# Kernel tuning notes

Hardware: AMD Instinct MI355X
Metric: run time of the kernel (lower is better)

## Reference

```python
import jax, jax.numpy as jnp
import numpy as np

B = 512       # batch_size
IN = 256      # input_size
H = 512       # hidden_size
OUT = 64      # output_size
N_PAIRS = B - 1   # number of H0 persistence deaths (connected components merges)
TOL = 1e-6    # rtol for torch.isclose
ATOL = 1e-8   # torch default atol
EPS = 0.0     # homology_eps
TARGET_P = 1.0
HOM_P = 1.0
COMP_P = 0.01

_IU = np.triu_indices(B, 1)  # condensed pdist indexing, static


def _mlp(batch, W1, b1, W2, b2, W3, b3, Wout, bout):
    # FeedForward: input->hidden, (n_layers-1) hidden->hidden, hidden->output, ReLU
    h = jax.nn.relu(batch @ W1 + b1)
    h = jax.nn.relu(h @ W2 + b2)
    h = jax.nn.relu(h @ W3 + b3)
    return h @ Wout + bout


def _pdist(y):
    # condensed euclidean pairwise distances, same ordering as torch F.pdist
    d = y[_IU[0]] - y[_IU[1]]                 # [P, OUT]
    return jnp.sqrt(jnp.sum(d * d, axis=-1))  # [P]


def setup_inputs() -> dict:
    key = jax.random.key(0)
    ks = jax.random.split(key, 8)
    batch = jax.random.normal(ks[0], (B, IN), jnp.float32)
    target = jax.random.normal(ks[1], (B, OUT), jnp.float32)
    W1 = jax.random.normal(ks[2], (IN, H), jnp.float32) / np.sqrt(IN)
    W2 = jax.random.normal(ks[3], (H, H), jnp.float32) / np.sqrt(H)
    W3 = jax.random.normal(ks[4], (H, H), jnp.float32) / np.sqrt(H)
    Wout = jax.random.normal(ks[5], (H, OUT), jnp.float32) / np.sqrt(H)
    b1 = jnp.zeros((H,), jnp.float32)
    b2 = jnp.zeros((H,), jnp.float32)
    b3 = jnp.zeros((H,), jnp.float32)
    bout = jnp.zeros((OUT,), jnp.float32)
    # persistence deaths = actual critical pdist values (from the external
    # Vietoris-Rips routine in the original); sample N_PAIRS distinct entries.
    y0 = _mlp(batch, W1, b1, W2, b2, W3, b3, Wout, bout)
    pd0 = np.asarray(_pdist(y0))
    idx = np.random.default_rng(0).choice(pd0.shape[0], N_PAIRS, replace=False)
    persistence_deaths = jnp.asarray(pd0[idx], jnp.float32)
    return {"batch": batch, "target": target,
            "W1": W1, "b1": b1, "W2": W2, "b2": b2, "W3": W3, "b3": b3,
            "Wout": Wout, "bout": bout,
            "persistence_deaths": persistence_deaths}


def reference(batch, target, W1, b1, W2, b2, W3, b3, Wout, bout, persistence_deaths):
    y = _mlp(batch, W1, b1, W2, b2, W3, b3, Wout, bout)   # [B, OUT]
    y_hom = y  # normalize_for_homology = False
    pd = _pdist(y_hom)                                     # [P]
    # vectorized indicator_death over all pairs (replaces per-pair Python loop)
    mask = jnp.any(jnp.isclose(pd[:, None], persistence_deaths[None, :],
                               rtol=TOL, atol=ATOL), axis=1)      # [P] bool
    # homology_dim=0: birth_pdist = 0; norm=1 of selected (death - 0 + eps)
    homology_loss = jnp.sum(jnp.abs(jnp.where(mask, pd + EPS, 0.0)))
    target_loss = jnp.mean((target - y) ** 2)
    compactness_loss = jnp.sum(jnp.abs(y - jnp.mean(y, axis=0, keepdims=True)))
    loss = TARGET_P * target_loss + HOM_P * homology_loss + COMP_P * compactness_loss
    return loss
```

## Files before the change

### kernel.cpp

```cpp
#include <hip/hip_runtime.h>

#define B_    512
#define IN_   256
#define H_    512
#define OUT_  64
#define NDEATH (B_ - 1)
#define NSORT  512
#define RTOL_ 1e-6
#define ATOL_ 1e-8
#define NBLK  256
#define NTHR  512
#define KT    32

typedef __attribute__((ext_vector_type(4))) double d4_t;

__device__ __forceinline__ void ast(double* p, double v) {
    __hip_atomic_store(p, v, __ATOMIC_RELAXED, __HIP_MEMORY_SCOPE_AGENT);
}
__device__ __forceinline__ double ald(const double* p) {
    return __hip_atomic_load(p, __ATOMIC_RELAXED, __HIP_MEMORY_SCOPE_AGENT);
}
__device__ __forceinline__ unsigned aldu(const unsigned* p) {
    return __hip_atomic_load(p, __ATOMIC_RELAXED, __HIP_MEMORY_SCOPE_AGENT);
}
__device__ __forceinline__ void aadd(unsigned* p) {
    __hip_atomic_fetch_add(p, 1u, __ATOMIC_RELAXED, __HIP_MEMORY_SCOPE_AGENT);
}

__device__ __forceinline__ void lbar() {
    asm volatile("s_waitcnt lgkmcnt(0)" ::: "memory");
    __builtin_amdgcn_s_barrier();
    asm volatile("" ::: "memory");
}

__device__ __forceinline__ void gbar(unsigned* cnt, unsigned nb) {
    __syncthreads();
    if (threadIdx.x == 0) {
        aadd(cnt);
        while (aldu(cnt) < nb) __builtin_amdgcn_s_sleep(1);
    }
    __syncthreads();
}

__device__ __forceinline__ void gbar2(unsigned* gslot, unsigned* root,
                                      int leader) {
    __syncthreads();
    if (threadIdx.x == 0) {
        aadd(gslot);
        if (leader) {
            while (aldu(gslot) < 16u) __builtin_amdgcn_s_sleep(1);
            aadd(root);
        }
        while (aldu(root) < 16u) __builtin_amdgcn_s_sleep(1);
    }
    __syncthreads();
}

__device__ void sort_windows(const float* __restrict__ deaths,
                             double* sd, double* slo, double* shi, int t) {
    if (t < NSORT) sd[t] = (t < NDEATH) ? (double)deaths[t] : 1e300;
    __syncthreads();
    for (int k = 2; k <= NSORT; k <<= 1) {
        for (int j = k >> 1; j > 0; j >>= 1) {
            if (t < 256) {
                int l = ((t & ~(j - 1)) << 1) | (t & (j - 1));
                int p = l + j;
                bool up = ((l & k) == 0);
                double a = sd[l], b = sd[p];
                if ((a > b) == up) { sd[l] = b; sd[p] = a; }
            }
            __syncthreads();
        }
    }
    if (t < NSORT) {
        double d = sd[t];
        double w = ATOL_ + RTOL_ * fabs(d);
        slo[t] = d - w;
        shi[t] = d + w;
    }
    __syncthreads();
}

template <typename TIN, bool RELU>
__device__ void gemm_dev(const TIN* __restrict__ A, const float* __restrict__ W,
                         const float* __restrict__ bias, double* __restrict__ C,
                         int N, int K, int tile, int t,
                         double (&As)[2][2][KT][33]) {
    const int lane  = t & 63;
    const int wave4 = (t >> 6) & 3;
    const int w2    = t >> 8;
    const int tg    = t & 255;
    const int wm    = wave4 & 1, wn = wave4 >> 1;
    const int nbx   = N >> 5;
    const int row0  = (tile / nbx) << 5;
    const int col0  = (tile % nbx) << 5;

    const int akk   = tg & 31;
    const int amm   = tg >> 5;
    const int kbase = w2 * (K >> 1);
    const int nkt   = K >> 6;

    const int mrow  = wm * 16 + (lane & 15);
    const int ncol  = wn * 16 + (lane & 15);
    const int kq    = lane >> 4;

    TIN   ar[3][4];
    float br[3][8];

    auto load_a = [&](int rs, int kt) {
        const int k0 = kbase + (kt << 5);
        #pragma unroll
        for (int p = 0; p < 4; ++p)
            ar[rs][p] = A[(size_t)(row0 + amm + 8 * p) * K + k0 + akk];
    };
    auto load_b = [&](int rs, int kt) {
        const int k0 = kbase + (kt << 5);
        const float* wp = W + (size_t)(k0 + kq) * N + col0 + ncol;
        #pragma unroll
        for (int ks = 0; ks < 8; ++ks)
            br[rs][ks] = wp[(size_t)(4 * ks) * N];
    };
    auto stage_a = [&](int rs, int buf) {
        #pragma unroll
        for (int p = 0; p < 4; ++p)
            As[w2][buf][akk][amm + 8 * p] = (double)ar[rs][p];
    };

    load_a(0, 0); load_b(0, 0);
    if (nkt > 1) { load_a(1, 1); load_b(1, 1); }
    if (nkt > 2) { load_a(2, 2); load_b(2, 2); }
    stage_a(0, 0);
    lbar();

    d4_t c4a = {0.0, 0.0, 0.0, 0.0};
    d4_t c4b = {0.0, 0.0, 0.0, 0.0};

    for (int kt = 0; kt < nkt; ++kt) {
        const int cur = kt & 1;
        const int rs  = kt % 3;
        #pragma unroll
        for (int ks = 0; ks < 4; ++ks) {
            double av = As[w2][cur][ks * 4 + kq][mrow];
            c4a = __builtin_amdgcn_mfma_f64_16x16x4f64(av, (double)br[rs][ks],
                                                       c4a, 0, 0, 0);
        }
        #pragma unroll
        for (int ks = 4; ks < 8; ++ks) {
            double av = As[w2][cur][ks * 4 + kq][mrow];
            c4b = __builtin_amdgcn_mfma_f64_16x16x4f64(av, (double)br[rs][ks],
                                                       c4b, 0, 0, 0);
        }
        if (kt + 3 < nkt) { load_a(rs, kt + 3); load_b(rs, kt + 3); }
        if (kt + 1 < nkt) stage_a((kt + 1) % 3, cur ^ 1);
        lbar();
    }

    d4_t c4 = c4a + c4b;

    double (*cEx)[16][17] = (double (*)[16][17])(&As[0][0][0][0]);
    const int r4 = (lane >> 4) * 4;
    if (w2 == 1) {
        #pragma unroll
        for (int r = 0; r < 4; ++r)
            cEx[wave4][r4 + r][lane & 15] = c4[r];
    }
    lbar();
    if (w2 == 0) {
        #pragma unroll
        for (int r = 0; r < 4; ++r) {
            int row = row0 + wm * 16 + r4 + r;
            int col = col0 + wn * 16 + (lane & 15);
            double v = c4[r] + cEx[wave4][r4 + r][lane & 15] + (double)bias[col];
            if (RELU) v = v > 0.0 ? v : 0.0;
            ast(&C[(size_t)row * N + col], v);
        }
    }
}

__device__ void mc_dev(const float* __restrict__ target,
                       const double* __restrict__ y,
                       double* __restrict__ t_part, double* __restrict__ c_part,
                       int c, int t) {
    const int wave = t >> 6, lane = t & 63;
    double v = y[(size_t)t * OUT_ + c];
    double s = v;
    for (int off = 32; off; off >>= 1) s += __shfl_down(s, off);
    __shared__ double swm[8];
    __shared__ double smean;
    if (lane == 0) swm[wave] = s;
    __syncthreads();
    if (t == 0) {
        double m = 0.0;
        #pragma unroll
        for (int w = 0; w < 8; ++w) m += swm[w];
        smean = m / (double)B_;
    }
    __syncthreads();
    double m = smean;
    double d = (double)target[(size_t)t * OUT_ + c] - v;
    double t_s = d * d;
    double c_s = fabs(v - m);
    for (int off = 32; off; off >>= 1) {
        t_s += __shfl_down(t_s, off);
        c_s += __shfl_down(c_s, off);
    }
    __shared__ double st[8], sc[8];
    if (lane == 0) { st[wave] = t_s; sc[wave] = c_s; }
    __syncthreads();
    if (t == 0) {
        double ts = 0.0, cs = 0.0;
        #pragma unroll
        for (int w = 0; w < 8; ++w) { ts += st[w]; cs += sc[w]; }
        ast(&t_part[c], ts);
        ast(&c_part[c], cs);
    }
}

__device__ __forceinline__ double pair_val(const double* __restrict__ yrow_s,
                                           const double* __restrict__ yj,
                                           const double* __restrict__ slo,
                                           const double* __restrict__ shi) {
    double s = 0.0;
    #pragma unroll
    for (int d = 0; d < OUT_; d += 2) {
        double2 v = *(const double2*)(yj + d);
        double d0 = yrow_s[d]     - v.x;
        double d1 = yrow_s[d + 1] - v.y;
        s = fma(d0, d0, s);
        s = fma(d1, d1, s);
    }
    double pd = sqrt(s);
    int pos = 0;
    #pragma unroll
    for (int step = NSORT / 2; step; step >>= 1) {
        if (slo[pos + step - 1] <= pd) pos += step;
    }
    bool m = (pos > 0) && (shi[pos - 1] >= pd);
    return m ? pd : 0.0;
}

__device__ void pdist_dev(const double* __restrict__ y,
                          double* __restrict__ hom_part, int bid, int t,
                          double* yA, double* yB,
                          const double* slo, const double* shi) {
    const int iA = bid;
    const int iB = 510 - bid;
    if (t < OUT_)            yA[t]        = y[(size_t)iA * OUT_ + t];
    else if (t < 2 * OUT_)   yB[t - OUT_] = y[(size_t)iB * OUT_ + (t - OUT_)];
    __syncthreads();

    double local = 0.0;
    for (int j = iA + 1 + t; j < B_; j += NTHR)
        local += pair_val(yA, y + (size_t)j * OUT_, slo, shi);
    if (iB != iA)
        for (int j = iB + 1 + t; j < B_; j += NTHR)
            local += pair_val(yB, y + (size_t)j * OUT_, slo, shi);

    for (int off = 32; off; off >>= 1) local += __shfl_down(local, off);
    __shared__ double sw[8];
    int wave = t >> 6, lane = t & 63;
    if (lane == 0) sw[wave] = local;
    __syncthreads();
    if (t == 0) {
        double s = 0.0;
        #pragma unroll
        for (int w = 0; w < 8; ++w) s += sw[w];
        ast(&hom_part[bid], s);
    }
}

__global__ __launch_bounds__(NTHR) void fused_k(
    const float* __restrict__ batch, const float* __restrict__ target,
    const float* __restrict__ W1, const float* __restrict__ b1,
    const float* __restrict__ W2, const float* __restrict__ b2,
    const float* __restrict__ W3, const float* __restrict__ b3,
    const float* __restrict__ Wout, const float* __restrict__ bout,
    const float* __restrict__ deaths, float* __restrict__ out,
    double* __restrict__ hA, double* __restrict__ hB,
    double* __restrict__ hC, double* __restrict__ yv,
    double* __restrict__ hom_part, double* __restrict__ t_part,
    double* __restrict__ c_part, unsigned* __restrict__ cnt,
    double* __restrict__ wbc) {
    const int bid = blockIdx.x;
    const int t   = threadIdx.x;
    const int g   = bid >> 4;
    const int c   = bid & 15;
    unsigned* gc  = cnt + g * 32;

    __shared__ double As[2][2][KT][33];
    __shared__ double slo[NSORT], shi[NSORT];
    __shared__ double yA[OUT_], yB[OUT_];
    double* sd = &As[0][0][0][0];

    gemm_dev<float,  true>(batch, W1, b1, hA, H_, IN_, bid, t, As);
    gbar(&gc[0], 16);
    gemm_dev<double, true>(hA, W2, b2, hB, H_, H_, bid, t, As);
    gbar(&gc[1], 16);
    gemm_dev<double, true>(hB, W3, b3, hC, H_, H_, bid, t, As);
    gbar(&gc[2], 16);

    if (c < 2) {
        gemm_dev<double, false>(hC, Wout, bout, yv, OUT_, H_, g * 2 + c, t, As);
    } else {
        sort_windows(deaths, sd, slo, shi, t);
        if (bid == 2 && t < NSORT) {
            ast(&wbc[t],         slo[t]);
            ast(&wbc[NSORT + t], shi[t]);
        }
    }

    gbar2(&gc[3], &cnt[512], c == 0);
    if (c < 2) {
        if (t < NSORT) {
            slo[t] = ald(&wbc[t]);
            shi[t] = ald(&wbc[NSORT + t]);
        }
        __syncthreads();
    }

    pdist_dev(yv, hom_part, bid, t, yA, yB, slo, shi);
    if (bid < OUT_) mc_dev(target, yv, t_part, c_part, bid, t);

    __syncthreads();
    if (t == 0) {
        aadd(&gc[4]);
        if (c == 0) {
            while (aldu(&gc[4]) < 16u) __builtin_amdgcn_s_sleep(1);
            aadd(&cnt[513]);
        }
    }
    if (bid != 0) return;
    if (t == 0)
        while (aldu(&cnt[513]) < 16u) __builtin_amdgcn_s_sleep(1);
    __syncthreads();

    {
        double h = 0.0, tp = 0.0, cp = 0.0;
        if (t < NBLK) h = ald(&hom_part[t]);
        if (t < OUT_) { tp = ald(&t_part[t]); cp = ald(&c_part[t]); }
        for (int off = 32; off; off >>= 1) {
            h  += __shfl_down(h,  off);
            tp += __shfl_down(tp, off);
            cp += __shfl_down(cp, off);
        }
        __shared__ double sh[8], stp[8], scp[8];
        int wave = t >> 6, lane = t & 63;
        if (lane == 0) { sh[wave] = h; stp[wave] = tp; scp[wave] = cp; }
        __syncthreads();
        if (t == 0) {
            double hs = 0.0, ts = 0.0, cs = 0.0;
            #pragma unroll
            for (int w = 0; w < 8; ++w) {
                hs += sh[w]; ts += stp[w]; cs += scp[w];
            }
            out[0] = (float)(ts / (double)(B_ * OUT_) + hs + 0.01 * cs);
        }
    }
}

extern "C" void kernel_launch(void* const* d_in, const int* in_sizes, int n_in,
                              void* d_out, int out_size, void* d_ws, size_t ws_size,
                              hipStream_t stream) {
    const float* batch  = (const float*)d_in[0];
    const float* target = (const float*)d_in[1];
    const float* W1     = (const float*)d_in[2];
    const float* b1     = (const float*)d_in[3];
    const float* W2     = (const float*)d_in[4];
    const float* b2     = (const float*)d_in[5];
    const float* W3     = (const float*)d_in[6];
    const float* b3     = (const float*)d_in[7];
    const float* Wout   = (const float*)d_in[8];
    const float* bout   = (const float*)d_in[9];
    const float* deaths = (const float*)d_in[10];
    float* out = (float*)d_out;

    double* hA       = (double*)d_ws;
    double* hB       = hA + (size_t)B_ * H_;
    double* hC       = hB + (size_t)B_ * H_;
    double* yv       = hC + (size_t)B_ * H_;
    double* hom_part = yv + (size_t)B_ * OUT_;
    double* t_part   = hom_part + NBLK;
    double* c_part   = t_part + OUT_;
    unsigned* cnt    = (unsigned*)(c_part + OUT_);
    double* wbc      = (double*)(cnt + 576);

    hipMemsetAsync(cnt, 0, 576 * sizeof(unsigned), stream);

    fused_k<<<dim3(NBLK), dim3(NTHR), 0, stream>>>(
        batch, target, W1, b1, W2, b2, W3, b3, Wout, bout, deaths, out,
        hA, hB, hC, yv, hom_part, t_part, c_part, cnt, wbc);
}
```

Baseline: 122.3 us.

## Split work across 512 blocks of 256 threads with 16-row GEMM tiles

Doubles the grid to 512 blocks and halves the threads per block. GEMM tiles shrink from 32x32 to 16x32, and the barrier groups grow from 16 to 32. The pdist, sort, mean/compactness and final reduction loops are remapped to the new thread count. The aim is to spread work over more CUs and cut per-block latency in the persistent fused kernel, at the cost of more global barrier participants and smaller MFMA tiles with less reuse.

```diff
diff --git a/kernel.cpp b/kernel.cpp
--- a/kernel.cpp
+++ b/kernel.cpp
@@ -8,8 +8,9 @@
 #define NSORT  512
 #define RTOL_ 1e-6
 #define ATOL_ 1e-8
-#define NBLK  256
-#define NTHR  512
+#define NBLK  512
+#define NTHR  256
+#define NGRP  32
 #define KT    32
 
 typedef __attribute__((ext_vector_type(4))) double d4_t;
@@ -51,32 +52,32 @@
             while (aldu(gslot) < 16u) __builtin_amdgcn_s_sleep(1);
             aadd(root);
         }
-        while (aldu(root) < 16u) __builtin_amdgcn_s_sleep(1);
+        while (aldu(root) < (unsigned)NGRP) __builtin_amdgcn_s_sleep(1);
     }
     __syncthreads();
 }
 
 __device__ void sort_windows(const float* __restrict__ deaths,
                              double* sd, double* slo, double* shi, int t) {
-    if (t < NSORT) sd[t] = (t < NDEATH) ? (double)deaths[t] : 1e300;
+    int i1 = t + 256;
+    sd[t]  = (t  < NDEATH) ? (double)deaths[t]  : 1e300;
+    sd[i1] = (i1 < NDEATH) ? (double)deaths[i1] : 1e300;
     __syncthreads();
     for (int k = 2; k <= NSORT; k <<= 1) {
         for (int j = k >> 1; j > 0; j >>= 1) {
-            if (t < 256) {
-                int l = ((t & ~(j - 1)) << 1) | (t & (j - 1));
-                int p = l + j;
-                bool up = ((l & k) == 0);
-                double a = sd[l], b = sd[p];
-                if ((a > b) == up) { sd[l] = b; sd[p] = a; }
-            }
+            int l = ((t & ~(j - 1)) << 1) | (t & (j - 1));
+            int p = l + j;
+            bool up = ((l & k) == 0);
+            double a = sd[l], b = sd[p];
+            if ((a > b) == up) { sd[l] = b; sd[p] = a; }
             __syncthreads();
         }
     }
-    if (t < NSORT) {
-        double d = sd[t];
+    for (int i = t; i < NSORT; i += 256) {
+        double d = sd[i];
         double w = ATOL_ + RTOL_ * fabs(d);
-        slo[t] = d - w;
-        shi[t] = d + w;
+        slo[i] = d - w;
+        shi[i] = d + w;
     }
     __syncthreads();
 }
@@ -85,24 +86,23 @@
 __device__ void gemm_dev(const TIN* __restrict__ A, const float* __restrict__ W,
                          const float* __restrict__ bias, double* __restrict__ C,
                          int N, int K, int tile, int t,
-                         double (&As)[2][2][KT][33]) {
+                         double (&As)[2][2][KT][17]) {
     const int lane  = t & 63;
-    const int wave4 = (t >> 6) & 3;
-    const int w2    = t >> 8;
-    const int tg    = t & 255;
-    const int wm    = wave4 & 1, wn = wave4 >> 1;
+    const int colq  = (t >> 6) & 1;
+    const int kw    = t >> 7;
     const int nbx   = N >> 5;
-    const int row0  = (tile / nbx) << 5;
+    const int row0  = (tile / nbx) << 4;
     const int col0  = (tile % nbx) << 5;
 
+    const int tg    = t & 127;
     const int akk   = tg & 31;
     const int amm   = tg >> 5;
-    const int kbase = w2 * (K >> 1);
+    const int kbase = kw * (K >> 1);
     const int nkt   = K >> 6;
 
-    const int mrow  = wm * 16 + (lane & 15);
-    const int ncol  = wn * 16 + (lane & 15);
+    const int mrow  = lane & 15;
     const int kq    = lane >> 4;
+    const int ncol  = colq * 16 + (lane & 15);
 
     TIN   ar[3][4];
     float br[3][8];
@@ -111,7 +111,7 @@
         const int k0 = kbase + (kt << 5);
         #pragma unroll
         for (int p = 0; p < 4; ++p)
-            ar[rs][p] = A[(size_t)(row0 + amm + 8 * p) * K + k0 + akk];
+            ar[rs][p] = A[(size_t)(row0 + amm + 4 * p) * K + k0 + akk];
     };
     auto load_b = [&](int rs, int kt) {
         const int k0 = kbase + (kt << 5);
@@ -123,7 +123,7 @@
     auto stage_a = [&](int rs, int buf) {
         #pragma unroll
         for (int p = 0; p < 4; ++p)
-            As[w2][buf][akk][amm + 8 * p] = (double)ar[rs][p];
+            As[kw][buf][akk][amm + 4 * p] = (double)ar[rs][p];
     };
 
     load_a(0, 0); load_b(0, 0);
@@ -140,13 +140,13 @@
         const int rs  = kt % 3;
         #pragma unroll
         for (int ks = 0; ks < 4; ++ks) {
-            double av = As[w2][cur][ks * 4 + kq][mrow];
+            double av = As[kw][cur][ks * 4 + kq][mrow];
             c4a = __builtin_amdgcn_mfma_f64_16x16x4f64(av, (double)br[rs][ks],
                                                        c4a, 0, 0, 0);
         }
         #pragma unroll
         for (int ks = 4; ks < 8; ++ks) {
-            double av = As[w2][cur][ks * 4 + kq][mrow];
+            double av = As[kw][cur][ks * 4 + kq][mrow];
             c4b = __builtin_amdgcn_mfma_f64_16x16x4f64(av, (double)br[rs][ks],
                                                        c4b, 0, 0, 0);
         }
@@ -159,18 +159,18 @@
 
     double (*cEx)[16][17] = (double (*)[16][17])(&As[0][0][0][0]);
     const int r4 = (lane >> 4) * 4;
-    if (w2 == 1) {
+    if (kw == 1) {
         #pragma unroll
         for (int r = 0; r < 4; ++r)
-            cEx[wave4][r4 + r][lane & 15] = c4[r];
+            cEx[colq][r4 + r][lane & 15] = c4[r];
     }
     lbar();
-    if (w2 == 0) {
+    if (kw == 0) {
         #pragma unroll
         for (int r = 0; r < 4; ++r) {
-            int row = row0 + wm * 16 + r4 + r;
-            int col = col0 + wn * 16 + (lane & 15);
-            double v = c4[r] + cEx[wave4][r4 + r][lane & 15] + (double)bias[col];
+            int row = row0 + r4 + r;
+            int col = col0 + colq * 16 + (lane & 15);
+            double v = c4[r] + cEx[colq][r4 + r][lane & 15] + (double)bias[col];
             if (RELU) v = v > 0.0 ? v : 0.0;
             ast(&C[(size_t)row * N + col], v);
         }
@@ -182,37 +182,31 @@
                        double* __restrict__ t_part, double* __restrict__ c_part,
                        int c, int t) {
     const int wave = t >> 6, lane = t & 63;
-    double v = y[(size_t)t * OUT_ + c];
-    double s = v;
+    double v0 = y[(size_t)t * OUT_ + c];
+    double v1 = y[(size_t)(t + 256) * OUT_ + c];
+    double s = v0 + v1;
     for (int off = 32; off; off >>= 1) s += __shfl_down(s, off);
-    __shared__ double swm[8];
+    __shared__ double swm[4];
     __shared__ double smean;
     if (lane == 0) swm[wave] = s;
     __syncthreads();
-    if (t == 0) {
-        double m = 0.0;
-        #pragma unroll
-        for (int w = 0; w < 8; ++w) m += swm[w];
-        smean = m / (double)B_;
-    }
+    if (t == 0) smean = (swm[0] + swm[1] + swm[2] + swm[3]) / (double)B_;
     __syncthreads();
     double m = smean;
-    double d = (double)target[(size_t)t * OUT_ + c] - v;
-    double t_s = d * d;
-    double c_s = fabs(v - m);
+    double d0 = (double)target[(size_t)t * OUT_ + c] - v0;
+    double d1 = (double)target[(size_t)(t + 256) * OUT_ + c] - v1;
+    double t_s = d0 * d0 + d1 * d1;
+    double c_s = fabs(v0 - m) + fabs(v1 - m);
     for (int off = 32; off; off >>= 1) {
         t_s += __shfl_down(t_s, off);
         c_s += __shfl_down(c_s, off);
     }
-    __shared__ double st[8], sc[8];
+    __shared__ double st[4], sc[4];
     if (lane == 0) { st[wave] = t_s; sc[wave] = c_s; }
     __syncthreads();
     if (t == 0) {
-        double ts = 0.0, cs = 0.0;
-        #pragma unroll
-        for (int w = 0; w < 8; ++w) { ts += st[w]; cs += sc[w]; }
-        ast(&t_part[c], ts);
-        ast(&c_part[c], cs);
+        ast(&t_part[c], st[0] + st[1] + st[2] + st[3]);
+        ast(&c_part[c], sc[0] + sc[1] + sc[2] + sc[3]);
     }
 }
 
@@ -243,30 +237,26 @@
                           double* __restrict__ hom_part, int bid, int t,
                           double* yA, double* yB,
                           const double* slo, const double* shi) {
-    const int iA = bid;
-    const int iB = 510 - bid;
+    const int iA  = bid >> 1;
+    const int iB  = 510 - iA;
+    const int par = bid & 1;
     if (t < OUT_)            yA[t]        = y[(size_t)iA * OUT_ + t];
     else if (t < 2 * OUT_)   yB[t - OUT_] = y[(size_t)iB * OUT_ + (t - OUT_)];
     __syncthreads();
 
     double local = 0.0;
-    for (int j = iA + 1 + t; j < B_; j += NTHR)
+    for (int j = iA + 1 + par + 2 * t; j < B_; j += 2 * NTHR)
         local += pair_val(yA, y + (size_t)j * OUT_, slo, shi);
     if (iB != iA)
-        for (int j = iB + 1 + t; j < B_; j += NTHR)
+        for (int j = iB + 1 + par + 2 * t; j < B_; j += 2 * NTHR)
             local += pair_val(yB, y + (size_t)j * OUT_, slo, shi);
 
     for (int off = 32; off; off >>= 1) local += __shfl_down(local, off);
-    __shared__ double sw[8];
+    __shared__ double sw[4];
     int wave = t >> 6, lane = t & 63;
     if (lane == 0) sw[wave] = local;
     __syncthreads();
-    if (t == 0) {
-        double s = 0.0;
-        #pragma unroll
-        for (int w = 0; w < 8; ++w) s += sw[w];
-        ast(&hom_part[bid], s);
-    }
+    if (t == 0) ast(&hom_part[bid], sw[0] + sw[1] + sw[2] + sw[3]);
 }
 
 __global__ __launch_bounds__(NTHR) void fused_k(
@@ -287,7 +277,7 @@
     const int c   = bid & 15;
     unsigned* gc  = cnt + g * 32;
 
-    __shared__ double As[2][2][KT][33];
+    __shared__ double As[2][2][KT][17];
     __shared__ double slo[NSORT], shi[NSORT];
     __shared__ double yA[OUT_], yB[OUT_];
     double* sd = &As[0][0][0][0];
@@ -303,17 +293,19 @@
         gemm_dev<double, false>(hC, Wout, bout, yv, OUT_, H_, g * 2 + c, t, As);
     } else {
         sort_windows(deaths, sd, slo, shi, t);
-        if (bid == 2 && t < NSORT) {
-            ast(&wbc[t],         slo[t]);
-            ast(&wbc[NSORT + t], shi[t]);
-        }
-    }
-
-    gbar2(&gc[3], &cnt[512], c == 0);
+        if (bid == 2) {
+            for (int i = t; i < NSORT; i += 256) {
+                ast(&wbc[i],         slo[i]);
+                ast(&wbc[NSORT + i], shi[i]);
+            }
+        }
+    }
+
+    gbar2(&gc[3], &cnt[1024], c == 0);
     if (c < 2) {
-        if (t < NSORT) {
-            slo[t] = ald(&wbc[t]);
-            shi[t] = ald(&wbc[NSORT + t]);
+        for (int i = t; i < NSORT; i += 256) {
+            slo[i] = ald(&wbc[i]);
+            shi[i] = ald(&wbc[NSORT + i]);
         }
         __syncthreads();
     }
@@ -326,33 +318,31 @@
         aadd(&gc[4]);
         if (c == 0) {
             while (aldu(&gc[4]) < 16u) __builtin_amdgcn_s_sleep(1);
-            aadd(&cnt[513]);
+            aadd(&cnt[1025]);
         }
     }
     if (bid != 0) return;
     if (t == 0)
-        while (aldu(&cnt[513]) < 16u) __builtin_amdgcn_s_sleep(1);
+        while (aldu(&cnt[1025]) < (unsigned)NGRP) __builtin_amdgcn_s_sleep(1);
     __syncthreads();
 
     {
-        double h = 0.0, tp = 0.0, cp = 0.0;
-        if (t < NBLK) h = ald(&hom_part[t]);
+        double h = ald(&hom_part[t]) + ald(&hom_part[t + 256]);
+        double tp = 0.0, cp = 0.0;
         if (t < OUT_) { tp = ald(&t_part[t]); cp = ald(&c_part[t]); }
         for (int off = 32; off; off >>= 1) {
             h  += __shfl_down(h,  off);
             tp += __shfl_down(tp, off);
             cp += __shfl_down(cp, off);
         }
-        __shared__ double sh[8], stp[8], scp[8];
+        __shared__ double sh[4], stp[4], scp[4];
         int wave = t >> 6, lane = t & 63;
         if (lane == 0) { sh[wave] = h; stp[wave] = tp; scp[wave] = cp; }
         __syncthreads();
         if (t == 0) {
-            double hs = 0.0, ts = 0.0, cs = 0.0;
-            #pragma unroll
-            for (int w = 0; w < 8; ++w) {
-                hs += sh[w]; ts += stp[w]; cs += scp[w];
-            }
+            double hs = sh[0]  + sh[1]  + sh[2]  + sh[3];
+            double ts = stp[0] + stp[1] + stp[2] + stp[3];
+            double cs = scp[0] + scp[1] + scp[2] + scp[3];
             out[0] = (float)(ts / (double)(B_ * OUT_) + hs + 0.01 * cs);
         }
     }
@@ -382,9 +372,9 @@
     double* t_part   = hom_part + NBLK;
     double* c_part   = t_part + OUT_;
     unsigned* cnt    = (unsigned*)(c_part + OUT_);
-    double* wbc      = (double*)(cnt + 576);
-
-    hipMemsetAsync(cnt, 0, 576 * sizeof(unsigned), stream);
+    double* wbc      = (double*)(cnt + 1088);
+
+    hipMemsetAsync(cnt, 0, 1088 * sizeof(unsigned), stream);
 
     fused_k<<<dim3(NBLK), dim3(NTHR), 0, stream>>>(
         batch, target, W1, b1, W2, b2, W3, b3, Wout, bout, deaths, out,
```

Measured after the change: 127.1 us. 1.04x slower.

## Load GEMM operands directly into registers and remap blocks to spread row groups

Applied to the files above, without the earlier changes.

The GEMM no longer stages A tiles through LDS with per-step barriers. Each lane now loads its A fragment straight from global memory into registers in MFMA operand layout, and the dimensions become template constants so the k-loop fully unrolls. The block-to-group mapping also changes so the 16 blocks of a row group are spread across block IDs, likely to distribute groups across XCDs. This removes the LDS traffic and barriers from the inner loop. In exchange, A loads become strided and less coalesced, and register pressure rises.

```diff
diff --git a/kernel.cpp b/kernel.cpp
--- a/kernel.cpp
+++ b/kernel.cpp
@@ -10,7 +10,6 @@
 #define ATOL_ 1e-8
 #define NBLK  256
 #define NTHR  512
-#define KT    32
 
 typedef __attribute__((ext_vector_type(4))) double d4_t;
 
@@ -25,12 +24,6 @@
 }
 __device__ __forceinline__ void aadd(unsigned* p) {
     __hip_atomic_fetch_add(p, 1u, __ATOMIC_RELAXED, __HIP_MEMORY_SCOPE_AGENT);
-}
-
-__device__ __forceinline__ void lbar() {
-    asm volatile("s_waitcnt lgkmcnt(0)" ::: "memory");
-    __builtin_amdgcn_s_barrier();
-    asm volatile("" ::: "memory");
 }
 
 __device__ __forceinline__ void gbar(unsigned* cnt, unsigned nb) {
@@ -81,96 +74,75 @@
     __syncthreads();
 }
 
-template <typename TIN, bool RELU>
+template <typename TIN, bool RELU, int N, int K>
 __device__ void gemm_dev(const TIN* __restrict__ A, const float* __restrict__ W,
                          const float* __restrict__ bias, double* __restrict__ C,
-                         int N, int K, int tile, int t,
-                         double (&As)[2][2][KT][33]) {
+                         int tile, int t, double (&cEx)[4][16][17]) {
     const int lane  = t & 63;
-    const int wave4 = (t >> 6) & 3;
-    const int w2    = t >> 8;
-    const int tg    = t & 255;
-    const int wm    = wave4 & 1, wn = wave4 >> 1;
-    const int nbx   = N >> 5;
+    const int chunk = (t >> 6) & 3;
+    const int wm    = chunk & 1;
+    const int wn    = chunk >> 1;
+    const int kw    = t >> 8;
+    constexpr int nbx = N >> 5;
     const int row0  = (tile / nbx) << 5;
     const int col0  = (tile % nbx) << 5;
 
-    const int akk   = tg & 31;
-    const int amm   = tg >> 5;
-    const int kbase = w2 * (K >> 1);
-    const int nkt   = K >> 6;
-
-    const int mrow  = wm * 16 + (lane & 15);
-    const int ncol  = wn * 16 + (lane & 15);
+    const int mrow  = lane & 15;
     const int kq    = lane >> 4;
-
-    TIN   ar[3][4];
-    float br[3][8];
-
-    auto load_a = [&](int rs, int kt) {
-        const int k0 = kbase + (kt << 5);
-        #pragma unroll
-        for (int p = 0; p < 4; ++p)
-            ar[rs][p] = A[(size_t)(row0 + amm + 8 * p) * K + k0 + akk];
+    const int kbase = kw * (K >> 1);
+    constexpr int nkt = K >> 6;
+
+    const TIN*   ap = A + (size_t)(row0 + wm * 16 + mrow) * K + kbase + kq;
+    const float* wp = W + (size_t)(kbase + kq) * N + col0 + wn * 16 + mrow;
+
+    double ar[3][8];
+    float  br[3][8];
+
+    auto load_ab = [&](int rs, int kt) {
+        const int k0 = kt << 5;
+        #pragma unroll
+        for (int i = 0; i < 8; ++i) {
+            ar[rs][i] = (double)ap[k0 + 4 * i];
+            br[rs][i] = wp[(size_t)(k0 + 4 * i) * N];
+        }
     };
-    auto load_b = [&](int rs, int kt) {
-        const int k0 = kbase + (kt << 5);
-        const float* wp = W + (size_t)(k0 + kq) * N + col0 + ncol;
-        #pragma unroll
-        for (int ks = 0; ks < 8; ++ks)
-            br[rs][ks] = wp[(size_t)(4 * ks) * N];
-    };
-    auto stage_a = [&](int rs, int buf) {
-        #pragma unroll
-        for (int p = 0; p < 4; ++p)
-            As[w2][buf][akk][amm + 8 * p] = (double)ar[rs][p];
-    };
-
-    load_a(0, 0); load_b(0, 0);
-    if (nkt > 1) { load_a(1, 1); load_b(1, 1); }
-    if (nkt > 2) { load_a(2, 2); load_b(2, 2); }
-    stage_a(0, 0);
-    lbar();
+
+    load_ab(0, 0);
+    if (nkt > 1) load_ab(1, 1);
+    if (nkt > 2) load_ab(2, 2);
 
     d4_t c4a = {0.0, 0.0, 0.0, 0.0};
     d4_t c4b = {0.0, 0.0, 0.0, 0.0};
 
+    #pragma unroll
     for (int kt = 0; kt < nkt; ++kt) {
-        const int cur = kt & 1;
-        const int rs  = kt % 3;
-        #pragma unroll
-        for (int ks = 0; ks < 4; ++ks) {
-            double av = As[w2][cur][ks * 4 + kq][mrow];
-            c4a = __builtin_amdgcn_mfma_f64_16x16x4f64(av, (double)br[rs][ks],
-                                                       c4a, 0, 0, 0);
-        }
-        #pragma unroll
-        for (int ks = 4; ks < 8; ++ks) {
-            double av = As[w2][cur][ks * 4 + kq][mrow];
-            c4b = __builtin_amdgcn_mfma_f64_16x16x4f64(av, (double)br[rs][ks],
-                                                       c4b, 0, 0, 0);
-        }
-        if (kt + 3 < nkt) { load_a(rs, kt + 3); load_b(rs, kt + 3); }
-        if (kt + 1 < nkt) stage_a((kt + 1) % 3, cur ^ 1);
-        lbar();
+        const int rs = kt % 3;
+        #pragma unroll
+        for (int ks = 0; ks < 4; ++ks)
+            c4a = __builtin_amdgcn_mfma_f64_16x16x4f64(ar[rs][ks],
+                      (double)br[rs][ks], c4a, 0, 0, 0);
+        #pragma unroll
+        for (int ks = 4; ks < 8; ++ks)
+            c4b = __builtin_amdgcn_mfma_f64_16x16x4f64(ar[rs][ks],
+                      (double)br[rs][ks], c4b, 0, 0, 0);
+        if (kt + 3 < nkt) load_ab(rs, kt + 3);
     }
 
     d4_t c4 = c4a + c4b;
 
-    double (*cEx)[16][17] = (double (*)[16][17])(&As[0][0][0][0]);
     const int r4 = (lane >> 4) * 4;
-    if (w2 == 1) {
+    if (kw == 1) {
         #pragma unroll
         for (int r = 0; r < 4; ++r)
-            cEx[wave4][r4 + r][lane & 15] = c4[r];
-    }
-    lbar();
-    if (w2 == 0) {
+            cEx[chunk][r4 + r][lane & 15] = c4[r];
+    }
+    __syncthreads();
+    if (kw == 0) {
         #pragma unroll
         for (int r = 0; r < 4; ++r) {
             int row = row0 + wm * 16 + r4 + r;
             int col = col0 + wn * 16 + (lane & 15);
-            double v = c4[r] + cEx[wave4][r4 + r][lane & 15] + (double)bias[col];
+            double v = c4[r] + cEx[chunk][r4 + r][lane & 15] + (double)bias[col];
             if (RELU) v = v > 0.0 ? v : 0.0;
             ast(&C[(size_t)row * N + col], v);
         }
@@ -283,27 +255,28 @@
     double* __restrict__ wbc) {
     const int bid = blockIdx.x;
     const int t   = threadIdx.x;
-    const int g   = bid >> 4;
-    const int c   = bid & 15;
+    const int g   = (bid & 7) | ((bid >> 7) << 3);
+    const int c   = (bid >> 3) & 15;
+    const int tile = g * 16 + c;
     unsigned* gc  = cnt + g * 32;
 
-    __shared__ double As[2][2][KT][33];
+    __shared__ double cEx[4][16][17];
     __shared__ double slo[NSORT], shi[NSORT];
     __shared__ double yA[OUT_], yB[OUT_];
-    double* sd = &As[0][0][0][0];
-
-    gemm_dev<float,  true>(batch, W1, b1, hA, H_, IN_, bid, t, As);
+    double* sd = &cEx[0][0][0];
+
+    gemm_dev<float,  true, H_, IN_>(batch, W1, b1, hA, tile, t, cEx);
     gbar(&gc[0], 16);
-    gemm_dev<double, true>(hA, W2, b2, hB, H_, H_, bid, t, As);
+    gemm_dev<double, true, H_, H_>(hA, W2, b2, hB, tile, t, cEx);
     gbar(&gc[1], 16);
-    gemm_dev<double, true>(hB, W3, b3, hC, H_, H_, bid, t, As);
+    gemm_dev<double, true, H_, H_>(hB, W3, b3, hC, tile, t, cEx);
     gbar(&gc[2], 16);
 
     if (c < 2) {
-        gemm_dev<double, false>(hC, Wout, bout, yv, OUT_, H_, g * 2 + c, t, As);
+        gemm_dev<double, false, OUT_, H_>(hC, Wout, bout, yv, g * 2 + c, t, cEx);
     } else {
         sort_windows(deaths, sd, slo, shi, t);
-        if (bid == 2 && t < NSORT) {
+        if (g == 0 && c == 2 && t < NSORT) {
             ast(&wbc[t],         slo[t]);
             ast(&wbc[NSORT + t], shi[t]);
         }
```

Measured after the change: 151.6 us. 1.24x slower.
